# Kernel optimization log

Hardware: AMD Instinct MI355X
Metric: run time of the kernel (lower is better)

The kernel has to match this reference:

```python
import jax, jax.numpy as jnp
import numpy as np

N_NODES = 50000
EPS = 1e-5


def gcn_conv(x, src, dst, ew, W, b):
    # PyG GCNConv (self-loops already appended by caller):
    # deg computed at target, symmetric normalization, linear, scatter-add.
    deg = jax.ops.segment_sum(ew, dst, num_segments=N_NODES)          # [N]
    dinv = jnp.where(deg > 0, jax.lax.rsqrt(jnp.maximum(deg, 1e-12)), 0.0)
    norm = dinv[src] * ew * dinv[dst]                                 # [E]
    h = x @ W                                                         # [N, F_out]
    msg = norm[:, None] * h[src]                                      # [E, F_out] gather
    out = jax.ops.segment_sum(msg, dst, num_segments=N_NODES)        # scatter-add
    return out + b


def layer_norm(x, gamma, beta):
    mu = jnp.mean(x, axis=-1, keepdims=True)
    var = jnp.mean(jnp.square(x - mu), axis=-1, keepdims=True)
    return (x - mu) * jax.lax.rsqrt(var + EPS) * gamma + beta


def setup_inputs() -> dict:
    key = jax.random.key(0)
    ks = jax.random.split(key, 8)
    N, E, D, H = N_NODES, 800000, 128, 256
    x = jax.random.normal(ks[0], (N, D), dtype=jnp.float32)
    edge_index = jax.random.randint(ks[1], (2, E), 0, N, dtype=jnp.int32)
    edge_weight = jax.random.uniform(ks[2], (E,), dtype=jnp.float32)
    # Glorot-ish init for weights, zeros for biases.
    W1 = jax.random.normal(ks[3], (D, H), dtype=jnp.float32) / np.sqrt(D)
    b1 = jnp.zeros((H,), dtype=jnp.float32)
    W2 = jax.random.normal(ks[4], (H, D), dtype=jnp.float32) / np.sqrt(H)
    b2 = jnp.zeros((D,), dtype=jnp.float32)
    gamma = jnp.ones((D,), dtype=jnp.float32)
    beta = jnp.zeros((D,), dtype=jnp.float32)
    return {"x": x, "edge_index": edge_index, "edge_weight": edge_weight,
            "W1": W1, "b1": b1, "W2": W2, "b2": b2,
            "gamma": gamma, "beta": beta}


def reference(x, edge_index, edge_weight, W1, b1, W2, b2, gamma, beta):
    N = x.shape[0]
    # Add self-loops with weight 1 (PyG default), shared by both layers.
    loops = jnp.arange(N, dtype=edge_index.dtype)
    src = jnp.concatenate([edge_index[0], loops])
    dst = jnp.concatenate([edge_index[1], loops])
    ew = jnp.concatenate([edge_weight, jnp.ones((N,), dtype=edge_weight.dtype)])

    h = gcn_conv(x, src, dst, ew, W1, b1)      # [N, hidden]
    h = jax.nn.relu(h)
    h = gcn_conv(h, src, dst, ew, W2, b2)      # [N, input_dim]
    return layer_norm(h, gamma, beta)
```

## Files before the change

kernel.cpp:

```cpp
#include <hip/hip_runtime.h>


#define TPB 256
#define SLOT 64

typedef __bf16 bf16;
typedef __bf16 bf16x2 __attribute__((ext_vector_type(2)));
typedef __bf16 bf16x4 __attribute__((ext_vector_type(4)));
typedef __bf16 bf16x8 __attribute__((ext_vector_type(8)));
typedef float  f32x4  __attribute__((ext_vector_type(4)));

__global__ void k_fill_prep(const int* __restrict__ dst, const int* __restrict__ src,
                            const float* __restrict__ ew,
                            unsigned long long* deg64,
                            unsigned int* __restrict__ csr, int E,
                            const float* __restrict__ x, bf16* __restrict__ x_bf,
                            const float* __restrict__ W1, bf16* __restrict__ W1T,
                            const float* __restrict__ W2, bf16* __restrict__ W2T,
                            int n4, int nw, int D, int H) {
  int i = blockIdx.x * TPB + threadIdx.x;
  if (i < E) {
    int d = dst[i];
    float wf = ew[i];
    unsigned long long add =
        ((unsigned long long)1 << 32) |
        (unsigned long long)(unsigned int)(wf * 65536.0f + 0.5f);
    unsigned long long old = atomicAdd(&deg64[d], add);
    unsigned int pos = (unsigned int)(old >> 32);
    if (pos < SLOT) {
      unsigned int wb = __float_as_uint((float)(bf16)wf) & 0xFFFF0000u;
      csr[((size_t)d << 6) | pos] = wb | (unsigned int)src[i];
    }
  }
  if (i < nw) {
    int r1 = i / H, c1 = i % H;
    W1T[(size_t)c1 * D + r1] = (bf16)W1[i];
    int r2 = i / D, c2 = i % D;
    W2T[(size_t)c2 * H + r2] = (bf16)W2[i];
  }
  if (i < n4) {
    float4 v = reinterpret_cast<const float4*>(x)[i];
    bf16x4 o;
    o.x = (bf16)v.x; o.y = (bf16)v.y; o.z = (bf16)v.z; o.w = (bf16)v.w;
    reinterpret_cast<bf16x4*>(x_bf)[i] = o;
  }
}

__global__ void k_deg(const unsigned long long* __restrict__ deg64,
                      float* __restrict__ dinv, int* __restrict__ cnt, int N) {
  int i = blockIdx.x * TPB + threadIdx.x;
  if (i < N) {
    unsigned long long v = deg64[i];
    unsigned int c = (unsigned int)(v >> 32);
    float d = 1.0f + (float)(v & 0xFFFFFFFFull) * (1.0f / 65536.0f);
    dinv[i] = rsqrtf(d);
    cnt[i] = (c < SLOT) ? (int)c : SLOT;
  }
}

__global__ __launch_bounds__(256) void k_gemm_mfma(
    const bf16* __restrict__ A, const bf16* __restrict__ BT,
    const float* __restrict__ bias, int relu, int M, int K, int NC,
    bf16* __restrict__ Cb) {
  const int l = threadIdx.x & 63, w = threadIdx.x >> 6;
  const int c = l & 15, g = l >> 4;
  const int m0 = blockIdx.x * 128 + w * 32;
  const int n0 = blockIdx.y * 64;

  int ra0 = m0 + c;       if (ra0 >= M) ra0 = M - 1;
  int ra1 = m0 + 16 + c;  if (ra1 >= M) ra1 = M - 1;
  const bf16* pa0 = A + (size_t)ra0 * K + g * 8;
  const bf16* pa1 = A + (size_t)ra1 * K + g * 8;
  const bf16* pb0 = BT + (size_t)(n0 + c) * K + g * 8;

  f32x4 acc[2][4] = {};
  for (int k0 = 0; k0 < K; k0 += 32) {
    bf16x8 a0 = *reinterpret_cast<const bf16x8*>(pa0 + k0);
    bf16x8 a1 = *reinterpret_cast<const bf16x8*>(pa1 + k0);
    bf16x8 b0 = *reinterpret_cast<const bf16x8*>(pb0 + k0);
    bf16x8 b1 = *reinterpret_cast<const bf16x8*>(pb0 + (size_t)16 * K + k0);
    bf16x8 b2 = *reinterpret_cast<const bf16x8*>(pb0 + (size_t)32 * K + k0);
    bf16x8 b3 = *reinterpret_cast<const bf16x8*>(pb0 + (size_t)48 * K + k0);
    acc[0][0] = __builtin_amdgcn_mfma_f32_16x16x32_bf16(b0, a0, acc[0][0], 0, 0, 0);
    acc[1][0] = __builtin_amdgcn_mfma_f32_16x16x32_bf16(b0, a1, acc[1][0], 0, 0, 0);
    acc[0][1] = __builtin_amdgcn_mfma_f32_16x16x32_bf16(b1, a0, acc[0][1], 0, 0, 0);
    acc[1][1] = __builtin_amdgcn_mfma_f32_16x16x32_bf16(b1, a1, acc[1][1], 0, 0, 0);
    acc[0][2] = __builtin_amdgcn_mfma_f32_16x16x32_bf16(b2, a0, acc[0][2], 0, 0, 0);
    acc[1][2] = __builtin_amdgcn_mfma_f32_16x16x32_bf16(b2, a1, acc[1][2], 0, 0, 0);
    acc[0][3] = __builtin_amdgcn_mfma_f32_16x16x32_bf16(b3, a0, acc[0][3], 0, 0, 0);
    acc[1][3] = __builtin_amdgcn_mfma_f32_16x16x32_bf16(b3, a1, acc[1][3], 0, 0, 0);
  }

#pragma unroll
  for (int mi = 0; mi < 2; ++mi) {
    int row = m0 + mi * 16 + c;
    if (row < M) {
#pragma unroll
      for (int ni = 0; ni < 4; ++ni) {
        int col0 = n0 + ni * 16 + g * 4;
        f32x4 v = acc[mi][ni];
        float4 bv = make_float4(0.f, 0.f, 0.f, 0.f);
        if (bias) bv = *reinterpret_cast<const float4*>(bias + col0);
        float o0 = v[0] + bv.x, o1 = v[1] + bv.y;
        float o2 = v[2] + bv.z, o3 = v[3] + bv.w;
        if (relu) {
          o0 = fmaxf(o0, 0.f); o1 = fmaxf(o1, 0.f);
          o2 = fmaxf(o2, 0.f); o3 = fmaxf(o3, 0.f);
        }
        bf16x4 ob;
        ob.x = (bf16)o0; ob.y = (bf16)o1; ob.z = (bf16)o2; ob.w = (bf16)o3;
        *reinterpret_cast<bf16x4*>(Cb + (size_t)row * NC + col0) = ob;
      }
    }
  }
}

#define UNPACK_EDGE(e, w, v)                                                   \
  float w = __uint_as_float((e) & 0xFFFF0000u) * dinv[(e) & 0xFFFFu];          \
  bf16x2 v = *reinterpret_cast<const bf16x2*>(h + (size_t)((e) & 0xFFFFu) * F + c2);

__global__ __launch_bounds__(256) void k_agg_x(
    const bf16* __restrict__ h, const float* __restrict__ dinv,
    const int* __restrict__ cnt, const unsigned int* __restrict__ csr,
    bf16* __restrict__ out, int N) {
  const int F = 128;
  int wid = threadIdx.x >> 6, lane = threadIdx.x & 63;
  int node = blockIdx.x * 4 + wid;
  if (node >= N) return;
  float di = dinv[node];
  int c2 = lane << 1;
  bf16x2 hv = *reinterpret_cast<const bf16x2*>(h + (size_t)node * F + c2);
  float nx = 0.f, ny = 0.f;
  const unsigned int* cp = csr + ((size_t)node << 6);
  int n = cnt[node];
  int j = 0;
  for (; j + 8 <= n; j += 8) {
    uint4 q0 = *reinterpret_cast<const uint4*>(cp + j);
    uint4 q1 = *reinterpret_cast<const uint4*>(cp + j + 4);
    UNPACK_EDGE(q0.x, w0, v0) UNPACK_EDGE(q0.y, w1, v1)
    UNPACK_EDGE(q0.z, w2, v2) UNPACK_EDGE(q0.w, w3, v3)
    UNPACK_EDGE(q1.x, w4, v4) UNPACK_EDGE(q1.y, w5, v5)
    UNPACK_EDGE(q1.z, w6, v6) UNPACK_EDGE(q1.w, w7, v7)
    nx += w0 * (float)v0.x + w1 * (float)v1.x + w2 * (float)v2.x + w3 * (float)v3.x
        + w4 * (float)v4.x + w5 * (float)v5.x + w6 * (float)v6.x + w7 * (float)v7.x;
    ny += w0 * (float)v0.y + w1 * (float)v1.y + w2 * (float)v2.y + w3 * (float)v3.y
        + w4 * (float)v4.y + w5 * (float)v5.y + w6 * (float)v6.y + w7 * (float)v7.y;
  }
  for (; j < n; ++j) {
    unsigned int e = cp[j];
    UNPACK_EDGE(e, w, v)
    nx += w * (float)v.x; ny += w * (float)v.y;
  }
  float sw = di * di;
  float ax = sw * (float)hv.x + di * nx;
  float ay = sw * (float)hv.y + di * ny;
  bf16x2 o; o.x = (bf16)ax; o.y = (bf16)ay;
  *reinterpret_cast<bf16x2*>(out + (size_t)node * F + c2) = o;
}

__global__ __launch_bounds__(256) void k_agg2_ln(
    const bf16* __restrict__ h, const float* __restrict__ dinv,
    const int* __restrict__ cnt, const unsigned int* __restrict__ csr,
    const float* __restrict__ b2, const float* __restrict__ gamma,
    const float* __restrict__ beta, float* __restrict__ out, int N) {
  const int F = 128;
  int wid = threadIdx.x >> 6, lane = threadIdx.x & 63;
  int node = blockIdx.x * 4 + wid;
  if (node >= N) return;
  float di = dinv[node];
  int c2 = lane << 1;
  float2 bb = *reinterpret_cast<const float2*>(b2 + c2);
  bf16x2 hv = *reinterpret_cast<const bf16x2*>(h + (size_t)node * F + c2);
  float nx = 0.f, ny = 0.f;
  const unsigned int* cp = csr + ((size_t)node << 6);
  int n = cnt[node];
  int j = 0;
  for (; j + 8 <= n; j += 8) {
    uint4 q0 = *reinterpret_cast<const uint4*>(cp + j);
    uint4 q1 = *reinterpret_cast<const uint4*>(cp + j + 4);
    UNPACK_EDGE(q0.x, w0, v0) UNPACK_EDGE(q0.y, w1, v1)
    UNPACK_EDGE(q0.z, w2, v2) UNPACK_EDGE(q0.w, w3, v3)
    UNPACK_EDGE(q1.x, w4, v4) UNPACK_EDGE(q1.y, w5, v5)
    UNPACK_EDGE(q1.z, w6, v6) UNPACK_EDGE(q1.w, w7, v7)
    nx += w0 * (float)v0.x + w1 * (float)v1.x + w2 * (float)v2.x + w3 * (float)v3.x
        + w4 * (float)v4.x + w5 * (float)v5.x + w6 * (float)v6.x + w7 * (float)v7.x;
    ny += w0 * (float)v0.y + w1 * (float)v1.y + w2 * (float)v2.y + w3 * (float)v3.y
        + w4 * (float)v4.y + w5 * (float)v5.y + w6 * (float)v6.y + w7 * (float)v7.y;
  }
  for (; j < n; ++j) {
    unsigned int e = cp[j];
    UNPACK_EDGE(e, w, v)
    nx += w * (float)v.x; ny += w * (float)v.y;
  }
  float sw = di * di;
  float ax = bb.x + sw * (float)hv.x + di * nx;
  float ay = bb.y + sw * (float)hv.y + di * ny;
  float s  = ax + ay;
  float ss = ax * ax + ay * ay;
  for (int m = 32; m > 0; m >>= 1) {
    s  += __shfl_xor(s, m, 64);
    ss += __shfl_xor(ss, m, 64);
  }
  float mu  = s * (1.0f / 128.0f);
  float var = ss * (1.0f / 128.0f) - mu * mu;
  float inv = rsqrtf(var + 1e-5f);
  float2 g  = *reinterpret_cast<const float2*>(gamma + c2);
  float2 be = *reinterpret_cast<const float2*>(beta + c2);
  float2 o;
  o.x = (ax - mu) * inv * g.x + be.x;
  o.y = (ay - mu) * inv * g.y + be.y;
  *reinterpret_cast<float2*>(out + (size_t)node * F + c2) = o;
}

extern "C" void kernel_launch(void* const* d_in, const int* in_sizes, int n_in,
                              void* d_out, int out_size, void* d_ws, size_t ws_size,
                              hipStream_t stream) {
  const float* x     = (const float*)d_in[0];
  const int*   ei    = (const int*)d_in[1];
  const float* ew    = (const float*)d_in[2];
  const float* W1    = (const float*)d_in[3];
  const float* b1    = (const float*)d_in[4];
  const float* W2    = (const float*)d_in[5];
  const float* b2    = (const float*)d_in[6];
  const float* gamma = (const float*)d_in[7];
  const float* beta  = (const float*)d_in[8];
  float* out = (float*)d_out;

  const int D = 128, H = 256;
  const int N = in_sizes[0] / D;
  const int E = in_sizes[2];
  const int* src = ei;
  const int* dst = ei + E;

  char* p = (char*)d_ws;
  auto carve = [&](size_t bytes) -> void* {
    void* r = (void*)p;
    p += (bytes + 255) & ~(size_t)255;
    return r;
  };
  float*              dinv  = (float*)carve((size_t)N * 4);
  int*                cnt   = (int*)  carve((size_t)N * 4);
  unsigned long long* deg64 = (unsigned long long*)carve((size_t)N * 8);
  unsigned int*       csr   = (unsigned int*)carve((size_t)N * SLOT * 4);
  bf16*               x_bf  = (bf16*) carve((size_t)N * D * 2);
  bf16*               axb   = (bf16*) carve((size_t)N * D * 2);
  bf16*               out1  = (bf16*) carve((size_t)N * H * 2);
  bf16*               h2    = (bf16*) carve((size_t)N * D * 2);
  bf16*               W1T   = (bf16*) carve((size_t)D * H * 2);
  bf16*               W2T   = (bf16*) carve((size_t)H * D * 2);

  const int gN = (N + TPB - 1) / TPB;
  const int n4 = N * D / 4;
  const int nw = D * H;
  const int gE = (E + TPB - 1) / TPB;
  const int gP = (n4 + TPB - 1) / TPB;
  const int gF = (gE > gP) ? gE : gP;

  hipMemsetAsync(deg64, 0, (size_t)N * 8, stream);
  k_fill_prep<<<gF, TPB, 0, stream>>>(dst, src, ew, deg64, csr, E,
                                      x, x_bf, W1, W1T, W2, W2T, n4, nw, D, H);
  k_deg<<<gN, TPB, 0, stream>>>(deg64, dinv, cnt, N);

  k_agg_x<<<(N + 3) / 4, TPB, 0, stream>>>(x_bf, dinv, cnt, csr, axb, N);
  dim3 g1((N + 127) / 128, H / 64);
  k_gemm_mfma<<<g1, TPB, 0, stream>>>(axb, W1T, b1, 1, N, D, H, out1);

  dim3 g2((N + 127) / 128, D / 64);
  k_gemm_mfma<<<g2, TPB, 0, stream>>>(out1, W2T, nullptr, 0, N, H, D, h2);
  k_agg2_ln<<<(N + 3) / 4, TPB, 0, stream>>>(h2, dinv, cnt, csr,
                                             b2, gamma, beta, out, N);
}
```

Baseline: 189.5 us.

## Fuse the two dense GEMMs into one kernel with hidden tile in LDS

Replaces the two separate MFMA GEMM launches with a single kernel that computes a 128-row tile of relu(AX·W1+b1) into shared memory and immediately multiplies it by W2. This removes the global write and re-read of the N×256 bf16 hidden activation and one kernel launch. In exchange, each block uses about 66KB of LDS and more accumulator registers, which lowers occupancy, and each block now covers all output columns, so there are fewer blocks.

```diff
diff --git a/kernel.cpp b/kernel.cpp
--- a/kernel.cpp
+++ b/kernel.cpp
@@ -55,63 +55,6 @@
     float d = 1.0f + (float)(v & 0xFFFFFFFFull) * (1.0f / 65536.0f);
     dinv[i] = rsqrtf(d);
     cnt[i] = (c < SLOT) ? (int)c : SLOT;
-  }
-}
-
-__global__ __launch_bounds__(256) void k_gemm_mfma(
-    const bf16* __restrict__ A, const bf16* __restrict__ BT,
-    const float* __restrict__ bias, int relu, int M, int K, int NC,
-    bf16* __restrict__ Cb) {
-  const int l = threadIdx.x & 63, w = threadIdx.x >> 6;
-  const int c = l & 15, g = l >> 4;
-  const int m0 = blockIdx.x * 128 + w * 32;
-  const int n0 = blockIdx.y * 64;
-
-  int ra0 = m0 + c;       if (ra0 >= M) ra0 = M - 1;
-  int ra1 = m0 + 16 + c;  if (ra1 >= M) ra1 = M - 1;
-  const bf16* pa0 = A + (size_t)ra0 * K + g * 8;
-  const bf16* pa1 = A + (size_t)ra1 * K + g * 8;
-  const bf16* pb0 = BT + (size_t)(n0 + c) * K + g * 8;
-
-  f32x4 acc[2][4] = {};
-  for (int k0 = 0; k0 < K; k0 += 32) {
-    bf16x8 a0 = *reinterpret_cast<const bf16x8*>(pa0 + k0);
-    bf16x8 a1 = *reinterpret_cast<const bf16x8*>(pa1 + k0);
-    bf16x8 b0 = *reinterpret_cast<const bf16x8*>(pb0 + k0);
-    bf16x8 b1 = *reinterpret_cast<const bf16x8*>(pb0 + (size_t)16 * K + k0);
-    bf16x8 b2 = *reinterpret_cast<const bf16x8*>(pb0 + (size_t)32 * K + k0);
-    bf16x8 b3 = *reinterpret_cast<const bf16x8*>(pb0 + (size_t)48 * K + k0);
-    acc[0][0] = __builtin_amdgcn_mfma_f32_16x16x32_bf16(b0, a0, acc[0][0], 0, 0, 0);
-    acc[1][0] = __builtin_amdgcn_mfma_f32_16x16x32_bf16(b0, a1, acc[1][0], 0, 0, 0);
-    acc[0][1] = __builtin_amdgcn_mfma_f32_16x16x32_bf16(b1, a0, acc[0][1], 0, 0, 0);
-    acc[1][1] = __builtin_amdgcn_mfma_f32_16x16x32_bf16(b1, a1, acc[1][1], 0, 0, 0);
-    acc[0][2] = __builtin_amdgcn_mfma_f32_16x16x32_bf16(b2, a0, acc[0][2], 0, 0, 0);
-    acc[1][2] = __builtin_amdgcn_mfma_f32_16x16x32_bf16(b2, a1, acc[1][2], 0, 0, 0);
-    acc[0][3] = __builtin_amdgcn_mfma_f32_16x16x32_bf16(b3, a0, acc[0][3], 0, 0, 0);
-    acc[1][3] = __builtin_amdgcn_mfma_f32_16x16x32_bf16(b3, a1, acc[1][3], 0, 0, 0);
-  }
-
-#pragma unroll
-  for (int mi = 0; mi < 2; ++mi) {
-    int row = m0 + mi * 16 + c;
-    if (row < M) {
-#pragma unroll
-      for (int ni = 0; ni < 4; ++ni) {
-        int col0 = n0 + ni * 16 + g * 4;
-        f32x4 v = acc[mi][ni];
-        float4 bv = make_float4(0.f, 0.f, 0.f, 0.f);
-        if (bias) bv = *reinterpret_cast<const float4*>(bias + col0);
-        float o0 = v[0] + bv.x, o1 = v[1] + bv.y;
-        float o2 = v[2] + bv.z, o3 = v[3] + bv.w;
-        if (relu) {
-          o0 = fmaxf(o0, 0.f); o1 = fmaxf(o1, 0.f);
-          o2 = fmaxf(o2, 0.f); o3 = fmaxf(o3, 0.f);
-        }
-        bf16x4 ob;
-        ob.x = (bf16)o0; ob.y = (bf16)o1; ob.z = (bf16)o2; ob.w = (bf16)o3;
-        *reinterpret_cast<bf16x4*>(Cb + (size_t)row * NC + col0) = ob;
-      }
-    }
   }
 }
 
@@ -156,6 +99,86 @@
   float ay = sw * (float)hv.y + di * ny;
   bf16x2 o; o.x = (bf16)ax; o.y = (bf16)ay;
   *reinterpret_cast<bf16x2*>(out + (size_t)node * F + c2) = o;
+}
+
+__global__ __launch_bounds__(256) void k_gemm12(
+    const bf16* __restrict__ A ,
+    const bf16* __restrict__ W1T , const float* __restrict__ b1,
+    const bf16* __restrict__ W2T ,
+    bf16* __restrict__ h2 , int M) {
+  const int D = 128, H = 256;
+  __shared__ bf16 o1s[128][264];
+  const int l = threadIdx.x & 63, w = threadIdx.x >> 6;
+  const int c = l & 15, g = l >> 4;
+  const int m0 = blockIdx.x * 128 + w * 32;
+
+  {
+    int ra0 = m0 + c;       if (ra0 >= M) ra0 = M - 1;
+    int ra1 = m0 + 16 + c;  if (ra1 >= M) ra1 = M - 1;
+    const bf16* pa0 = A + (size_t)ra0 * D + g * 8;
+    const bf16* pa1 = A + (size_t)ra1 * D + g * 8;
+#pragma unroll
+    for (int pass = 0; pass < 2; ++pass) {
+      const int n0 = pass * 128;
+      f32x4 acc[2][8] = {};
+      for (int k0 = 0; k0 < D; k0 += 32) {
+        bf16x8 a0 = *reinterpret_cast<const bf16x8*>(pa0 + k0);
+        bf16x8 a1 = *reinterpret_cast<const bf16x8*>(pa1 + k0);
+#pragma unroll
+        for (int ni = 0; ni < 8; ++ni) {
+          const bf16* pb = W1T + (size_t)(n0 + ni * 16 + c) * D + k0 + g * 8;
+          bf16x8 b = *reinterpret_cast<const bf16x8*>(pb);
+          acc[0][ni] = __builtin_amdgcn_mfma_f32_16x16x32_bf16(b, a0, acc[0][ni], 0, 0, 0);
+          acc[1][ni] = __builtin_amdgcn_mfma_f32_16x16x32_bf16(b, a1, acc[1][ni], 0, 0, 0);
+        }
+      }
+#pragma unroll
+      for (int mi = 0; mi < 2; ++mi) {
+        int lrow = w * 32 + mi * 16 + c;
+#pragma unroll
+        for (int ni = 0; ni < 8; ++ni) {
+          int col0 = n0 + ni * 16 + g * 4;
+          float4 bv = *reinterpret_cast<const float4*>(b1 + col0);
+          f32x4 v = acc[mi][ni];
+          float o0 = fmaxf(v[0] + bv.x, 0.f), o1 = fmaxf(v[1] + bv.y, 0.f);
+          float o2 = fmaxf(v[2] + bv.z, 0.f), o3 = fmaxf(v[3] + bv.w, 0.f);
+          bf16x4 ob;
+          ob.x = (bf16)o0; ob.y = (bf16)o1; ob.z = (bf16)o2; ob.w = (bf16)o3;
+          *reinterpret_cast<bf16x4*>(&o1s[lrow][col0]) = ob;
+        }
+      }
+    }
+  }
+  __syncthreads();
+
+  {
+    f32x4 acc[2][8] = {};
+    for (int k0 = 0; k0 < H; k0 += 32) {
+      bf16x8 a0 = *reinterpret_cast<const bf16x8*>(&o1s[w * 32 + c][k0 + g * 8]);
+      bf16x8 a1 = *reinterpret_cast<const bf16x8*>(&o1s[w * 32 + 16 + c][k0 + g * 8]);
+#pragma unroll
+      for (int ni = 0; ni < 8; ++ni) {
+        const bf16* pb = W2T + (size_t)(ni * 16 + c) * H + k0 + g * 8;
+        bf16x8 b = *reinterpret_cast<const bf16x8*>(pb);
+        acc[0][ni] = __builtin_amdgcn_mfma_f32_16x16x32_bf16(b, a0, acc[0][ni], 0, 0, 0);
+        acc[1][ni] = __builtin_amdgcn_mfma_f32_16x16x32_bf16(b, a1, acc[1][ni], 0, 0, 0);
+      }
+    }
+#pragma unroll
+    for (int mi = 0; mi < 2; ++mi) {
+      int row = m0 + mi * 16 + c;
+      if (row < M) {
+#pragma unroll
+        for (int ni = 0; ni < 8; ++ni) {
+          int col0 = ni * 16 + g * 4;
+          f32x4 v = acc[mi][ni];
+          bf16x4 ob;
+          ob.x = (bf16)v[0]; ob.y = (bf16)v[1]; ob.z = (bf16)v[2]; ob.w = (bf16)v[3];
+          *reinterpret_cast<bf16x4*>(h2 + (size_t)row * D + col0) = ob;
+        }
+      }
+    }
+  }
 }
 
 __global__ __launch_bounds__(256) void k_agg2_ln(
@@ -244,7 +267,6 @@
   unsigned int*       csr   = (unsigned int*)carve((size_t)N * SLOT * 4);
   bf16*               x_bf  = (bf16*) carve((size_t)N * D * 2);
   bf16*               axb   = (bf16*) carve((size_t)N * D * 2);
-  bf16*               out1  = (bf16*) carve((size_t)N * H * 2);
   bf16*               h2    = (bf16*) carve((size_t)N * D * 2);
   bf16*               W1T   = (bf16*) carve((size_t)D * H * 2);
   bf16*               W2T   = (bf16*) carve((size_t)H * D * 2);
@@ -262,11 +284,8 @@
   k_deg<<<gN, TPB, 0, stream>>>(deg64, dinv, cnt, N);
 
   k_agg_x<<<(N + 3) / 4, TPB, 0, stream>>>(x_bf, dinv, cnt, csr, axb, N);
-  dim3 g1((N + 127) / 128, H / 64);
-  k_gemm_mfma<<<g1, TPB, 0, stream>>>(axb, W1T, b1, 1, N, D, H, out1);
-
-  dim3 g2((N + 127) / 128, D / 64);
-  k_gemm_mfma<<<g2, TPB, 0, stream>>>(out1, W2T, nullptr, 0, N, H, D, h2);
+  k_gemm12<<<(N + 127) / 128, TPB, 0, stream>>>(axb, W1T, b1, W2T, h2, N);
+
   k_agg2_ln<<<(N + 3) / 4, TPB, 0, stream>>>(h2, dinv, cnt, csr,
                                              b2, gamma, beta, out, N);
 }
```

Result: faster. 179.6 us (-5.2%).
